# Kernel tuning notes

Hardware: AMD Instinct MI355X
Metric: run time of the kernel (lower is better)

The kernel has to match this reference:

```python
import jax, jax.numpy as jnp
import numpy as np

B, N = 256, 256


def greedy_hard_perm(soft_perm):
    # soft_perm: (B, N, N). Sequential greedy masked-argmax assignment, vectorized over batch.
    Bn, Nn, _ = soft_perm.shape
    NEG = jnp.finfo(soft_perm.dtype).min
    b_idx = jnp.arange(Bn)

    def step(carry, _):
        scores, hard, row_mask, col_mask = carry
        # mask out already-assigned rows/cols (in-place masked_fill_ in torch -> carried scores)
        scores = jnp.where(row_mask[:, :, None], NEG, scores)
        scores = jnp.where(col_mask[:, None, :], NEG, scores)
        flat_idx = jnp.argmax(scores.reshape(Bn, -1), axis=1)  # (B,)
        r = flat_idx // Nn
        c = flat_idx % Nn
        hard = hard.at[b_idx, r, c].set(1.0)
        row_mask = row_mask.at[b_idx, r].set(True)
        col_mask = col_mask.at[b_idx, c].set(True)
        return (scores, hard, row_mask, col_mask), None

    init = (
        soft_perm,
        jnp.zeros_like(soft_perm),
        jnp.zeros((Bn, Nn), dtype=bool),
        jnp.zeros((Bn, Nn), dtype=bool),
    )
    (_, hard, _, _), _ = jax.lax.scan(step, init, None, length=Nn)
    return hard


def setup_inputs() -> dict:
    key = jax.random.key(0)
    logits = jax.random.normal(key, (B, N, N), dtype=jnp.float32)
    # realistic soft permutation: row-stochastic scores
    soft_perm = jax.nn.softmax(logits, axis=-1)
    return {"soft_perm": soft_perm}


def reference(soft_perm):
    # hard perm carries no gradient (built from constant 1.0 writes in torch)
    hard = greedy_hard_perm(jax.lax.stop_gradient(soft_perm))
    # straight-through estimator: forward = hard, backward = identity through soft
    return hard + soft_perm - jax.lax.stop_gradient(soft_perm)
```

## Files before the change

### kernel.cpp

```cpp
#include <hip/hip_runtime.h>
#include <math.h>

#define NEGINF (-INFINITY)

template <int CTRL>
__device__ __forceinline__ float dppmax(float x) {
    int xi = __float_as_int(x);
    int yi = __builtin_amdgcn_update_dpp(xi, xi, CTRL, 0xf, 0xf, false);
    return fmaxf(x, __int_as_float(yi));
}

__device__ __forceinline__ float wave_max64(float x) {
    x = dppmax<0x111>(x);
    x = dppmax<0x112>(x);
    x = dppmax<0x114>(x);
    x = dppmax<0x118>(x);
    x = dppmax<0x142>(x);
    x = dppmax<0x143>(x);
    return __int_as_float(__builtin_amdgcn_readlane(__float_as_int(x), 63));
}

__device__ __forceinline__ void wave_argmax(float v, int idx, float& out_v, int& out_idx) {
    float mv = wave_max64(v);
    unsigned long long mask = __ballot(v == mv);
    int ln = (int)__builtin_ctzll(mask);
    int bi = __builtin_amdgcn_readlane(idx, ln);
    unsigned long long rest = mask & (mask - 1);
    if (rest) {
        while (rest) {
            int l2 = (int)__builtin_ctzll(rest); rest &= rest - 1;
            int b2 = __builtin_amdgcn_readlane(idx, l2);
            if (b2 < bi) bi = b2;
        }
    }
    out_v = mv; out_idx = bi;
}

__global__ __launch_bounds__(64, 1) void greedy_perm_kernel(
        const float* __restrict__ soft, float* __restrict__ out) {
    const int b = blockIdx.x;
    const int lane = threadIdx.x;
    const size_t base = (size_t)b << 16;
    const float* sc = soft + base;
    float* ob = out + base;

    float v[4];
    int   c[4];

#pragma unroll
    for (int j = 0; j < 4; ++j) { v[j] = NEGINF; c[j] = 0; }

    const float4 zero4 = make_float4(0.f, 0.f, 0.f, 0.f);

    for (int k = 0; k < 64; k += 4) {
        float4 w[4][4];
#pragma unroll
        for (int j = 0; j < 4; ++j) {
            const float4* rp = (const float4*)(sc + (size_t)(j * 64 + lane) * 256);
#pragma unroll
            for (int kk = 0; kk < 4; ++kk) w[j][kk] = rp[k + kk];
        }
#pragma unroll
        for (int j = 0; j < 4; ++j) {
            float4* op = (float4*)(ob + (size_t)(j * 64 + lane) * 256);
#pragma unroll
            for (int kk = 0; kk < 4; ++kk) op[k + kk] = zero4;
        }
#pragma unroll
        for (int j = 0; j < 4; ++j) {
#pragma unroll
            for (int kk = 0; kk < 4; ++kk) {
                const float4 ww = w[j][kk];
                const int bc = 4 * (k + kk);
                if (ww.x > v[j]) { v[j] = ww.x; c[j] = bc + 0; }
                if (ww.y > v[j]) { v[j] = ww.y; c[j] = bc + 1; }
                if (ww.z > v[j]) { v[j] = ww.z; c[j] = bc + 2; }
                if (ww.w > v[j]) { v[j] = ww.w; c[j] = bc + 3; }
            }
        }
    }

    __threadfence_block();

    unsigned int colmask = 0;

    for (int step = 0; step < 256; ++step) {
        float bv = v[0];
        int   bf = (lane << 8) | (c[0] & 255);
#pragma unroll
        for (int j = 1; j < 4; ++j) {
            int f = ((j * 64 + lane) << 8) | (c[j] & 255);
            if (v[j] > bv || (v[j] == bv && f < bf)) { bv = v[j]; bf = f; }
        }
        float gv; int gf;
        wave_argmax(bv, bf, gv, gf);
        const int r  = gf >> 8;
        const int cc = gf & 255;

        if (lane == 0) ob[gf] = 1.0f;
        if (lane == (r & 63)) { v[r >> 6] = NEGINF; c[r >> 6] = 300; }
        if (lane == (cc >> 2)) colmask |= 1u << (cc & 3);

#pragma unroll
        for (int j = 0; j < 4; ++j) {
            unsigned long long m = __ballot(c[j] == cc);
            while (m) {
                const int ln = (int)__builtin_ctzll(m); m &= m - 1;
                const int row = j * 64 + ln;
                float4 w = *(const float4*)(sc + (size_t)row * 256 + lane * 4);
                float m0 = (colmask & 1u) ? NEGINF : w.x;
                float m1 = (colmask & 2u) ? NEGINF : w.y;
                float m2 = (colmask & 4u) ? NEGINF : w.z;
                float m3 = (colmask & 8u) ? NEGINF : w.w;
                float lv = m0; int lf = 4 * lane + 0;
                if (m1 > lv) { lv = m1; lf = 4 * lane + 1; }
                if (m2 > lv) { lv = m2; lf = 4 * lane + 2; }
                if (m3 > lv) { lv = m3; lf = 4 * lane + 3; }
                float rv; int rf;
                wave_argmax(lv, lf, rv, rf);
                if (lane == ln) { v[j] = rv; c[j] = rf; }
            }
        }
    }
}

extern "C" void kernel_launch(void* const* d_in, const int* in_sizes, int n_in,
                              void* d_out, int out_size, void* d_ws, size_t ws_size,
                              hipStream_t stream) {
    const float* soft = (const float*)d_in[0];
    float* out = (float*)d_out;
    const int n_batches = in_sizes[0] >> 16;

    greedy_perm_kernel<<<n_batches, 64, 0, stream>>>(soft, out);
}
```

Measured before the change: 327.7 us.

## Cache bf16-truncated scores in LDS and pack argmax keys into u32

Stores the upper 16 bits of every score in a 128KB shared-memory table with a rotated-column layout, and keeps each row's best candidate as a packed 32-bit key (score bits plus inverted flat index). The wave argmax becomes a single unsigned DPP max, with no ballot-based tie resolution except when truncated keys collide; only then are exact values re-read from global memory. Row recomputation after a column is taken reads from LDS instead of global memory, and taken columns are marked by zeroing LDS entries rather than kept in a per-lane column mask. In exchange it adds LDS traffic and tie-handling complexity, and the 128KB allocation may limit occupancy, though it is one 64-thread block per batch anyway.

After: 366.4 us. +11.8%, slower.

```diff
diff --git a/kernel.cpp b/kernel.cpp
--- a/kernel.cpp
+++ b/kernel.cpp
@@ -4,121 +4,187 @@
 #define NEGINF (-INFINITY)
 
 template <int CTRL>
-__device__ __forceinline__ float dppmax(float x) {
-    int xi = __float_as_int(x);
-    int yi = __builtin_amdgcn_update_dpp(xi, xi, CTRL, 0xf, 0xf, false);
-    return fmaxf(x, __int_as_float(yi));
-}
-
-__device__ __forceinline__ float wave_max64(float x) {
-    x = dppmax<0x111>(x);
-    x = dppmax<0x112>(x);
-    x = dppmax<0x114>(x);
-    x = dppmax<0x118>(x);
-    x = dppmax<0x142>(x);
-    x = dppmax<0x143>(x);
-    return __int_as_float(__builtin_amdgcn_readlane(__float_as_int(x), 63));
-}
-
-__device__ __forceinline__ void wave_argmax(float v, int idx, float& out_v, int& out_idx) {
-    float mv = wave_max64(v);
-    unsigned long long mask = __ballot(v == mv);
-    int ln = (int)__builtin_ctzll(mask);
-    int bi = __builtin_amdgcn_readlane(idx, ln);
-    unsigned long long rest = mask & (mask - 1);
-    if (rest) {
-        while (rest) {
-            int l2 = (int)__builtin_ctzll(rest); rest &= rest - 1;
-            int b2 = __builtin_amdgcn_readlane(idx, l2);
-            if (b2 < bi) bi = b2;
-        }
+__device__ __forceinline__ unsigned dppmax_u32(unsigned x) {
+    unsigned y = (unsigned)__builtin_amdgcn_update_dpp((int)x, (int)x, CTRL, 0xf, 0xf, false);
+    return x > y ? x : y;
+}
+__device__ __forceinline__ unsigned wave_max_u32(unsigned x) {
+    x = dppmax_u32<0x111>(x);
+    x = dppmax_u32<0x112>(x);
+    x = dppmax_u32<0x114>(x);
+    x = dppmax_u32<0x118>(x);
+    x = dppmax_u32<0x142>(x);
+    x = dppmax_u32<0x143>(x);
+    return (unsigned)__builtin_amdgcn_readlane((int)x, 63);
+}
+
+__device__ __forceinline__ unsigned resolve_exact(bool has, unsigned fbits, unsigned flat) {
+    unsigned long long m = __ballot(has);
+    unsigned bb = 0u, bf = 0xFFFFFFFFu;
+    while (m) {
+        int ln = (int)__builtin_ctzll(m); m &= m - 1;
+        unsigned b2 = (unsigned)__builtin_amdgcn_readlane((int)fbits, ln);
+        unsigned f2 = (unsigned)__builtin_amdgcn_readlane((int)flat, ln);
+        if (b2 > bb || (b2 == bb && f2 < bf)) { bb = b2; bf = f2; }
     }
-    out_v = mv; out_idx = bi;
+    return bf;
 }
 
 __global__ __launch_bounds__(64, 1) void greedy_perm_kernel(
         const float* __restrict__ soft, float* __restrict__ out) {
-    const int b = blockIdx.x;
+    __shared__ unsigned short lk[65536];
     const int lane = threadIdx.x;
-    const size_t base = (size_t)b << 16;
+    const size_t base = (size_t)blockIdx.x << 16;
     const float* sc = soft + base;
     float* ob = out + base;
 
-    float v[4];
-    int   c[4];
-
-#pragma unroll
-    for (int j = 0; j < 4; ++j) { v[j] = NEGINF; c[j] = 0; }
-
-    const float4 zero4 = make_float4(0.f, 0.f, 0.f, 0.f);
-
-    for (int k = 0; k < 64; k += 4) {
-        float4 w[4][4];
+    unsigned hkey[4];
+
+    {
+        float v1[4]; int c1[4];
+#pragma unroll
+        for (int j = 0; j < 4; ++j) { v1[j] = NEGINF; c1[j] = 0; }
+        const float4 zero4 = make_float4(0.f, 0.f, 0.f, 0.f);
+        for (int k = 0; k < 64; k += 4) {
+            float4 w[4][4];
+#pragma unroll
+            for (int j = 0; j < 4; ++j) {
+                const float4* rp = (const float4*)(sc + (size_t)(j * 64 + lane) * 256);
+#pragma unroll
+                for (int kk = 0; kk < 4; ++kk) w[j][kk] = rp[k + kk];
+            }
+#pragma unroll
+            for (int j = 0; j < 4; ++j) {
+                float4* op = (float4*)(ob + (size_t)(j * 64 + lane) * 256);
+#pragma unroll
+                for (int kk = 0; kk < 4; ++kk) op[k + kk] = zero4;
+            }
+#pragma unroll
+            for (int j = 0; j < 4; ++j) {
+                const int r = j * 64 + lane;
+#pragma unroll
+                for (int kk = 0; kk < 4; ++kk) {
+                    const float4 ww = w[j][kk];
+                    const int bc = 4 * (k + kk);
+                    if (ww.x > v1[j]) { v1[j] = ww.x; c1[j] = bc + 0; }
+                    if (ww.y > v1[j]) { v1[j] = ww.y; c1[j] = bc + 1; }
+                    if (ww.z > v1[j]) { v1[j] = ww.z; c1[j] = bc + 2; }
+                    if (ww.w > v1[j]) { v1[j] = ww.w; c1[j] = bc + 3; }
+                    ushort4 st;
+                    st.x = (unsigned short)(__float_as_uint(ww.x) >> 16);
+                    st.y = (unsigned short)(__float_as_uint(ww.y) >> 16);
+                    st.z = (unsigned short)(__float_as_uint(ww.z) >> 16);
+                    st.w = (unsigned short)(__float_as_uint(ww.w) >> 16);
+                    const int idx = (r << 8) + ((bc + (r << 2)) & 255);
+                    *(ushort4*)&lk[idx] = st;
+                }
+            }
+        }
 #pragma unroll
         for (int j = 0; j < 4; ++j) {
-            const float4* rp = (const float4*)(sc + (size_t)(j * 64 + lane) * 256);
-#pragma unroll
-            for (int kk = 0; kk < 4; ++kk) w[j][kk] = rp[k + kk];
-        }
+            const unsigned flat = (unsigned)(((j * 64 + lane) << 8) | c1[j]);
+            hkey[j] = ((__float_as_uint(v1[j]) >> 16) << 16) | (0xFFFFu ^ flat);
+        }
+    }
+    __threadfence_block();
+
+    for (int step = 0; step < 256; ++step) {
+        unsigned W = hkey[0];
+        W = W > hkey[1] ? W : hkey[1];
+        W = W > hkey[2] ? W : hkey[2];
+        W = W > hkey[3] ? W : hkey[3];
+        W = wave_max_u32(W);
+        const unsigned k16s = W >> 16;
+        unsigned flat = (~W) & 0xFFFFu;
+
+        {
+            int cnt = (int)(hkey[0] >> 16 == k16s) + (int)(hkey[1] >> 16 == k16s)
+                    + (int)(hkey[2] >> 16 == k16s) + (int)(hkey[3] >> 16 == k16s);
+            unsigned long long b1 = __ballot(cnt >= 1);
+            if (((b1 & (b1 - 1)) != 0ull) || __ballot(cnt >= 2)) {
+                bool has = false; unsigned bb = 0u, bfl = 0xFFFFu;
+#pragma unroll
+                for (int j = 0; j < 4; ++j) {
+                    if (hkey[j] >> 16 == k16s) {
+                        const unsigned fl = (~hkey[j]) & 0xFFFFu;
+                        const unsigned bits = __float_as_uint(sc[fl]);
+                        if (!has || bits > bb || (bits == bb && fl < bfl)) {
+                            bb = bits; bfl = fl; has = true;
+                        }
+                    }
+                }
+                flat = resolve_exact(has, bb, bfl);
+            }
+        }
+        const int r = (int)(flat >> 8), cc = (int)(flat & 255u);
+
+        if (lane == 0) ob[flat] = 1.0f;
+
+        {
+            const int jw = r >> 6, ow = r & 63;
+#pragma unroll
+            for (int j = 0; j < 4; ++j)
+                if (j == jw && lane == ow) hkey[j] = 0u;
+        }
+
 #pragma unroll
         for (int j = 0; j < 4; ++j) {
-            float4* op = (float4*)(ob + (size_t)(j * 64 + lane) * 256);
-#pragma unroll
-            for (int kk = 0; kk < 4; ++kk) op[k + kk] = zero4;
-        }
-#pragma unroll
-        for (int j = 0; j < 4; ++j) {
-#pragma unroll
-            for (int kk = 0; kk < 4; ++kk) {
-                const float4 ww = w[j][kk];
-                const int bc = 4 * (k + kk);
-                if (ww.x > v[j]) { v[j] = ww.x; c[j] = bc + 0; }
-                if (ww.y > v[j]) { v[j] = ww.y; c[j] = bc + 1; }
-                if (ww.z > v[j]) { v[j] = ww.z; c[j] = bc + 2; }
-                if (ww.w > v[j]) { v[j] = ww.w; c[j] = bc + 3; }
-            }
-        }
-    }
-
-    __threadfence_block();
-
-    unsigned int colmask = 0;
-
-    for (int step = 0; step < 256; ++step) {
-        float bv = v[0];
-        int   bf = (lane << 8) | (c[0] & 255);
-#pragma unroll
-        for (int j = 1; j < 4; ++j) {
-            int f = ((j * 64 + lane) << 8) | (c[j] & 255);
-            if (v[j] > bv || (v[j] == bv && f < bf)) { bv = v[j]; bf = f; }
-        }
-        float gv; int gf;
-        wave_argmax(bv, bf, gv, gf);
-        const int r  = gf >> 8;
-        const int cc = gf & 255;
-
-        if (lane == 0) ob[gf] = 1.0f;
-        if (lane == (r & 63)) { v[r >> 6] = NEGINF; c[r >> 6] = 300; }
-        if (lane == (cc >> 2)) colmask |= 1u << (cc & 3);
-
-#pragma unroll
-        for (int j = 0; j < 4; ++j) {
-            unsigned long long m = __ballot(c[j] == cc);
-            while (m) {
-                const int ln = (int)__builtin_ctzll(m); m &= m - 1;
-                const int row = j * 64 + ln;
-                float4 w = *(const float4*)(sc + (size_t)row * 256 + lane * 4);
-                float m0 = (colmask & 1u) ? NEGINF : w.x;
-                float m1 = (colmask & 2u) ? NEGINF : w.y;
-                float m2 = (colmask & 4u) ? NEGINF : w.z;
-                float m3 = (colmask & 8u) ? NEGINF : w.w;
-                float lv = m0; int lf = 4 * lane + 0;
-                if (m1 > lv) { lv = m1; lf = 4 * lane + 1; }
-                if (m2 > lv) { lv = m2; lf = 4 * lane + 2; }
-                if (m3 > lv) { lv = m3; lf = 4 * lane + 3; }
-                float rv; int rf;
-                wave_argmax(lv, lf, rv, rf);
-                if (lane == ln) { v[j] = rv; c[j] = rf; }
+            const int rr = j * 64 + lane;
+            lk[(rr << 8) + ((cc + (rr << 2)) & 255)] = 0;
+        }
+
+        if (step == 255) break;
+
+        const bool s0 = hkey[0] && (((~hkey[0]) & 255u) == (unsigned)cc);
+        const bool s1 = hkey[1] && (((~hkey[1]) & 255u) == (unsigned)cc);
+        const bool s2 = hkey[2] && (((~hkey[2]) & 255u) == (unsigned)cc);
+        const bool s3 = hkey[3] && (((~hkey[3]) & 255u) == (unsigned)cc);
+        if (__ballot(s0 | s1 | s2 | s3)) {
+#pragma unroll
+            for (int j = 0; j < 4; ++j) {
+                const bool sj = j == 0 ? s0 : j == 1 ? s1 : j == 2 ? s2 : s3;
+                unsigned long long m = __ballot(sj);
+                while (m) {
+                    const int ln = (int)__builtin_ctzll(m); m &= m - 1;
+                    const int rp = j * 64 + ln;
+                    const ushort4 kk4 = *(const ushort4*)&lk[(rp << 8) + 4 * lane];
+                    const int colbase = (4 * lane - (rp << 2)) & 255;
+                    const unsigned flb = (unsigned)((rp << 8) | colbase);
+                    unsigned ck = ((unsigned)kk4.x << 16) | (0xFFFFu ^ (flb + 0u));
+                    unsigned c1k = ((unsigned)kk4.y << 16) | (0xFFFFu ^ (flb + 1u));
+                    unsigned c2k = ((unsigned)kk4.z << 16) | (0xFFFFu ^ (flb + 2u));
+                    unsigned c3k = ((unsigned)kk4.w << 16) | (0xFFFFu ^ (flb + 3u));
+                    ck = ck > c1k ? ck : c1k;
+                    ck = ck > c2k ? ck : c2k;
+                    ck = ck > c3k ? ck : c3k;
+                    const unsigned H = wave_max_u32(ck);
+                    const unsigned k16r = H >> 16;
+                    unsigned newhead = H;
+                    const int cnt = (int)(kk4.x == k16r) + (int)(kk4.y == k16r)
+                                  + (int)(kk4.z == k16r) + (int)(kk4.w == k16r);
+                    unsigned long long t1 = __ballot(cnt >= 1);
+                    if (((t1 & (t1 - 1)) != 0ull) || __ballot(cnt >= 2)) {
+                        bool has = false; unsigned bb = 0u, bfl = 0xFFFFu;
+                        const unsigned short ks[4] = {kk4.x, kk4.y, kk4.z, kk4.w};
+#pragma unroll
+                        for (int q = 0; q < 4; ++q) {
+                            if (ks[q] == k16r) {
+                                const unsigned fl = flb + (unsigned)q;
+                                const unsigned bits = __float_as_uint(sc[fl]);
+                                if (!has || bits > bb || (bits == bb && fl < bfl)) {
+                                    bb = bits; bfl = fl; has = true;
+                                }
+                            }
+                        }
+                        const unsigned rflat = resolve_exact(has, bb, bfl);
+                        newhead = (k16r << 16) | (0xFFFFu ^ rflat);
+                    }
+                    if (lane == ln) {
+#pragma unroll
+                        for (int j2 = 0; j2 < 4; ++j2)
+                            if (j2 == j) hkey[j2] = newhead;
+                    }
+                }
             }
         }
     }
@@ -130,6 +196,5 @@
     const float* soft = (const float*)d_in[0];
     float* out = (float*)d_out;
     const int n_batches = in_sizes[0] >> 16;
-
     greedy_perm_kernel<<<n_batches, 64, 0, stream>>>(soft, out);
 }
```
